# Performance work log

Measured on AMD Instinct MI355X. Metric: run time of the kernel, lower is better.

Reference implementation:

```python
import jax, jax.numpy as jnp
import numpy as np

EMBED_DIM = 1024
NUM_HEADS = 16
HEAD_DIM = EMBED_DIM // NUM_HEADS


def setup_inputs() -> dict:
    key = jax.random.key(0)
    k1, k2, k3, k4, k5 = jax.random.split(key, 5)
    B, T, C = 2, 2048, EMBED_DIM
    s = 1.0 / np.sqrt(C)
    return {
        "x": jax.random.normal(k1, (B, T, C), dtype=jnp.float32),
        "W_qkv": jax.random.normal(k2, (C, 3 * C), dtype=jnp.float32) * s,
        "b_qkv": jnp.zeros((3 * C,), dtype=jnp.float32),
        "W_out": jax.random.normal(k3, (C, C), dtype=jnp.float32) * s,
        "b_out": jnp.zeros((C,), dtype=jnp.float32),
    }


def reference(x, W_qkv, b_qkv, W_out, b_out):
    B, T, C = x.shape
    H, D = NUM_HEADS, HEAD_DIM
    qkv = x @ W_qkv + b_qkv                       # [B, T, 3C]
    q, k, v = jnp.split(qkv, 3, axis=-1)
    # [B, H, T, D]
    q = q.reshape(B, T, H, D).transpose(0, 2, 1, 3)
    k = k.reshape(B, T, H, D).transpose(0, 2, 1, 3)
    v = v.reshape(B, T, H, D).transpose(0, 2, 1, 3)
    scores = jnp.einsum("bhqd,bhkd->bhqk", q, k) / np.sqrt(D)  # [B,H,T,T]
    causal = jnp.tril(jnp.ones((T, T), dtype=bool))
    scores = jnp.where(causal[None, None], scores, -jnp.inf)
    weights = jax.nn.softmax(scores, axis=-1)
    out = jnp.einsum("bhqk,bhkd->bhqd", weights, v)  # [B,H,T,D]
    out = out.transpose(0, 2, 1, 3).reshape(B, T, C)
    return out @ W_out + b_out
```

## Files before the change

### kernel.cpp

```cpp
#include <hip/hip_runtime.h>
#include <stdint.h>

typedef unsigned short u16t;
typedef __attribute__((ext_vector_type(8))) short bf16x8;
typedef __attribute__((ext_vector_type(4))) float f32x4;

#define DEV __device__ __forceinline__

DEV u16t f2bf(float f) {
  union { float f; unsigned u; } v; v.f = f;
  unsigned r = v.u + 0x7FFFu + ((v.u >> 16) & 1u);
  return (u16t)(r >> 16);
}

DEV unsigned cvtpk(float a, float b) {
  unsigned r;
  asm("v_cvt_pk_bf16_f32 %0, %1, %2" : "=v"(r) : "v"(a), "v"(b));
  return r;
}

DEV void glds16(const void* g, void* l) {
  __builtin_amdgcn_global_load_lds((const __attribute__((address_space(1))) void*)g,
                                   (__attribute__((address_space(3))) void*)l, 16, 0, 0);
}

DEV void transpose_tile(const float* __restrict__ src, u16t* __restrict__ dst,
                        int R, int C, int c0, int r0, u16t (*tile)[65]) {
  int tid = threadIdx.x;
#pragma unroll
  for (int i = 0; i < 16; i++) {
    int idx = tid + i * 256;
    int r = idx >> 6, c = idx & 63;
    tile[c][r] = f2bf(src[(size_t)(r0 + r) * C + (c0 + c)]);
  }
  __syncthreads();
#pragma unroll
  for (int i = 0; i < 16; i++) {
    int idx = tid + i * 256;
    int rr = idx >> 6, cc = idx & 63;
    dst[(size_t)(c0 + rr) * R + (r0 + cc)] = tile[rr][cc];
  }
}

__global__ __launch_bounds__(256) void k_prep(const float* __restrict__ x,
                                              u16t* __restrict__ xb,
                                              const float* __restrict__ Wqkv,
                                              u16t* __restrict__ wqkvT,
                                              const float* __restrict__ Wout,
                                              u16t* __restrict__ woutT) {
  __shared__ u16t tile[64][65];
  const int bid = blockIdx.x;
  if (bid < 2048) {
    int i = (bid * 256 + threadIdx.x) * 8;
    const float4* p = (const float4*)(x + i);
    float4 a = p[0], b = p[1];
    union { u16t h[8]; int4 v; } o;
    o.h[0] = f2bf(a.x); o.h[1] = f2bf(a.y); o.h[2] = f2bf(a.z); o.h[3] = f2bf(a.w);
    o.h[4] = f2bf(b.x); o.h[5] = f2bf(b.y); o.h[6] = f2bf(b.z); o.h[7] = f2bf(b.w);
    *(int4*)(xb + i) = o.v;
  } else if (bid < 2816) {
    int b2 = bid - 2048;
    transpose_tile(Wqkv, wqkvT, 1024, 3072, (b2 % 48) * 64, (b2 / 48) * 64, tile);
  } else {
    int b3 = bid - 2816;
    transpose_tile(Wout, woutT, 1024, 1024, (b3 & 15) * 64, (b3 >> 4) * 64, tile);
  }
}

template <int K, int BM, int BN>
DEV void gemm_mainloop_t(const u16t* __restrict__ A, const u16t* __restrict__ Bt,
                         int m0, int n0, u16t* ldsA, u16t* ldsB,
                         f32x4 (&acc)[BM / 32][BN / 32]) {
  constexpr int MF = BM / 32, NF = BN / 32;
  const int tid = threadIdx.x;
  const int lane = tid & 63;
  const int wid = tid >> 6;
  const int wm = wid >> 1, wn = wid & 1;
#pragma unroll
  for (int i = 0; i < MF; i++)
#pragma unroll
    for (int j = 0; j < NF; j++) acc[i][j] = f32x4{0.f, 0.f, 0.f, 0.f};

  char* lA = (char*)ldsA;
  char* lB = (char*)ldsB;

  for (int k0 = 0; k0 < K; k0 += 32) {
#pragma unroll
    for (int j = wid; j < BM / 16; j += 4) {
      int g = j * 64 + lane;
      int row = g >> 2;
      int cb = (g & 3) * 16;
      glds16((const char*)(A + (size_t)(m0 + row) * K + k0) + cb, lA + j * 1024);
    }
#pragma unroll
    for (int j = wid; j < BN / 16; j += 4) {
      int g = j * 64 + lane;
      int row = g >> 2;
      int cb = (g & 3) * 16;
      glds16((const char*)(Bt + (size_t)(n0 + row) * K + k0) + cb, lB + j * 1024);
    }
    __syncthreads();
    bf16x8 af[MF], bfr[NF];
    const int lr = lane & 15;
    const int ko = (lane >> 4) * 8;
#pragma unroll
    for (int f = 0; f < MF; f++)
      af[f] = *(const bf16x8*)(ldsA + (wm * (BM / 2) + f * 16 + lr) * 32 + ko);
#pragma unroll
    for (int f = 0; f < NF; f++)
      bfr[f] = *(const bf16x8*)(ldsB + (wn * (BN / 2) + f * 16 + lr) * 32 + ko);
#pragma unroll
    for (int i = 0; i < MF; i++)
#pragma unroll
      for (int j = 0; j < NF; j++)
        acc[i][j] = __builtin_amdgcn_mfma_f32_16x16x32_bf16(af[i], bfr[j], acc[i][j], 0, 0, 0);
    __syncthreads();
  }
}

__global__ __launch_bounds__(256) void k_gemm_qkv(const u16t* __restrict__ xb,
                                                  const u16t* __restrict__ wt,
                                                  const float* __restrict__ bias,
                                                  u16t* __restrict__ q,
                                                  u16t* __restrict__ kk,
                                                  u16t* __restrict__ vt) {
  __shared__ alignas(16) char pool[32768];
  u16t* ldsA = (u16t*)pool;
  u16t* ldsB = (u16t*)(pool + 8192);
  const int m0 = blockIdx.x * 128, n0 = blockIdx.y * 128;
  f32x4 acc[4][4];
  gemm_mainloop_t<1024, 128, 128>(xb, wt, m0, n0, ldsA, ldsB, acc);

  const int lane = threadIdx.x & 63, wid = threadIdx.x >> 6;
  const int wm = wid >> 1, wn = wid & 1;
  const int nbase = n0 + wn * 64;
  const int which = nbase >> 10;
  const int hb = (nbase & 1023) >> 6;
  const int bb = m0 >> 11;
  const int t0 = (m0 & 2047) + wm * 64;
  const int bh = bb * 16 + hb;
  u16t* eb = (u16t*)(pool + wid * 8192);
#pragma unroll
  for (int fm = 0; fm < 4; fm++) {
#pragma unroll
    for (int fn = 0; fn < 4; fn++) {
      float bv = bias[nbase + fn * 16 + (lane & 15)];
#pragma unroll
      for (int i = 0; i < 4; i++) {
        int t_loc = fm * 16 + (lane >> 4) * 4 + i;
        int d_loc = fn * 16 + (lane & 15);
        float v = acc[fm][fn][i] + bv;
        if (which == 2) eb[d_loc * 64 + t_loc] = f2bf(v);
        else            eb[t_loc * 64 + d_loc] = f2bf(v);
      }
    }
  }
  asm volatile("s_waitcnt lgkmcnt(0)" ::: "memory");
  u16t* dst;
  size_t base, rowstride;
  if (which == 2) { dst = vt; base = (size_t)bh * 64 * 2048 + t0; rowstride = 2048; }
  else { dst = (which == 0) ? q : kk; base = ((size_t)bh * 2048 + t0) * 64; rowstride = 64; }
#pragma unroll
  for (int it = 0; it < 8; it++) {
    int g = it * 64 + lane;
    int r = g >> 3;
    int ce = (g & 7) * 8;
    *(int4*)(dst + base + (size_t)r * rowstride + ce) = *(const int4*)(eb + r * 64 + ce);
  }
}

__global__ __launch_bounds__(128) void k_attn(const u16t* __restrict__ q,
                                              const u16t* __restrict__ kk,
                                              const u16t* __restrict__ vt,
                                              u16t* __restrict__ attn) {
  __shared__ u16t ldsK[64 * 64];
  __shared__ u16t ldsV[64 * 64];
  __shared__ u16t ldsP[2][16 * 64];
  const int lin = blockIdx.x;
  const int swz = (lin & 7) * 128 + (lin >> 3);
  const int p = swz & 31;
  const int bh = swz >> 5;
  const int t_lo = p, t_hi = 63 - p;
  const int lo_last = t_lo >> 1, hi_last = t_hi >> 1;
  const int tid = threadIdx.x;
  const int lane = tid & 63, wid = tid >> 6;
  const int lr = lane & 15, lg = lane >> 4;
  const size_t hbase = (size_t)bh * 2048 * 64;
  const size_t vbase = (size_t)bh * 64 * 2048;
  const float NINF = -__builtin_inff();
  const float CEXP = 0.1803368801111204f;
  const float NMC  = -48.0f * 0.1803368801111204f;

  bf16x8 qlo[2], qhi[2];
  {
    const u16t* qp  = q + hbase + (size_t)(t_lo * 32 + wid * 16 + lr) * 64 + lg * 8;
    const u16t* qp2 = q + hbase + (size_t)(t_hi * 32 + wid * 16 + lr) * 64 + lg * 8;
#pragma unroll
    for (int ks = 0; ks < 2; ks++) {
      qlo[ks] = *(const bf16x8*)(qp + ks * 32);
      qhi[ks] = *(const bf16x8*)(qp2 + ks * 32);
    }
  }

  f32x4 olo[4], ohi[4];
#pragma unroll
  for (int i = 0; i < 4; i++) {
    olo[i] = f32x4{0.f, 0.f, 0.f, 0.f};
    ohi[i] = f32x4{0.f, 0.f, 0.f, 0.f};
  }
  float llo = 0.f, lhi = 0.f;

  u16t* pb = ldsP[wid];

  auto stage = [&](int kt) {
#pragma unroll
    for (int j = 0; j < 4; j++) {
      int g = j * 128 + tid;
      int r = g >> 3;
      int cb = (g & 7) * 16;
      int sc = cb ^ ((r & 7) << 4);
      glds16((const char*)(kk + hbase + (size_t)(kt * 64 + r) * 64) + sc,
             (char*)ldsK + j * 2048 + wid * 1024);
      glds16((const char*)(vt + vbase + (size_t)r * 2048 + kt * 64) + sc,
             (char*)ldsV + j * 2048 + wid * 1024);
    }
  };

  auto compute = [&](bool diag, int moff, const bf16x8* qf, f32x4* o, float& l_part) {
    const char* K = (const char*)ldsK;
    const char* V = (const char*)ldsV;
    float sv[4][4];
    __builtin_amdgcn_s_setprio(1);
#pragma unroll
    for (int f = 0; f < 4; f++) {
      f32x4 s = f32x4{0.f, 0.f, 0.f, 0.f};
#pragma unroll
      for (int ks = 0; ks < 2; ks++) {
        int row = f * 16 + lr;
        int cb = ks * 64 + lg * 16;
        bf16x8 kf = *(const bf16x8*)(K + row * 128 + (cb ^ ((row & 7) << 4)));
        s = __builtin_amdgcn_mfma_f32_16x16x32_bf16(kf, qf[ks], s, 0, 0, 0);
      }
#pragma unroll
      for (int i = 0; i < 4; i++) sv[f][i] = s[i];
    }
    __builtin_amdgcn_s_setprio(0);
    if (diag) {
      int qr = moff + wid * 16 + lr;
#pragma unroll
      for (int f = 0; f < 4; f++)
#pragma unroll
        for (int i = 0; i < 4; i++)
          if (f * 16 + lg * 4 + i > qr) sv[f][i] = NINF;
    }
    float ps[4][4];
    float fs[4];
#pragma unroll
    for (int f = 0; f < 4; f++) {
#pragma unroll
      for (int i = 0; i < 4; i++)
        ps[f][i] = exp2f(__builtin_fmaf(sv[f][i], CEXP, NMC));
      fs[f] = (ps[f][0] + ps[f][1]) + (ps[f][2] + ps[f][3]);
    }
    l_part += (fs[0] + fs[1]) + (fs[2] + fs[3]);
#pragma unroll
    for (int f = 0; f < 4; f++) {
      union { unsigned u[2]; uint2 v; } pk;
      pk.u[0] = cvtpk(ps[f][0], ps[f][1]);
      pk.u[1] = cvtpk(ps[f][2], ps[f][3]);
      int cby = (f * 32 + lg * 8) ^ ((lr & 7) << 4);
      *(uint2*)((char*)pb + lr * 128 + cby) = pk.v;
    }
    asm volatile("s_waitcnt lgkmcnt(0)" ::: "memory");
    __builtin_amdgcn_s_setprio(1);
#pragma unroll
    for (int ks = 0; ks < 2; ks++) {
      int cb = ks * 64 + lg * 16;
      bf16x8 pf = *(const bf16x8*)((const char*)pb + lr * 128 + (cb ^ ((lr & 7) << 4)));
#pragma unroll
      for (int df = 0; df < 4; df++) {
        int vrow = df * 16 + lr;
        bf16x8 vf = *(const bf16x8*)(V + vrow * 128 + (cb ^ ((vrow & 7) << 4)));
        o[df] = __builtin_amdgcn_mfma_f32_16x16x32_bf16(vf, pf, o[df], 0, 0, 0);
      }
    }
    __builtin_amdgcn_s_setprio(0);
  };

  for (int kt = 0; kt <= hi_last; kt++) {
    stage(kt);
    __syncthreads();
    compute(kt == hi_last, (t_hi & 1) << 5, qhi, ohi, lhi);
    if (kt <= lo_last) compute(kt == lo_last, (t_lo & 1) << 5, qlo, olo, llo);
    __syncthreads();
  }

  const int bb = bh >> 4, h = bh & 15;
  auto epi = [&](int qt, const f32x4* o, float l_part) {
    float l = l_part;
    l += __shfl_xor(l, 16);
    l += __shfl_xor(l, 32);
    float rinv = 1.0f / l;
    int t = qt * 32 + wid * 16 + lr;
    size_t rowb = ((size_t)bb * 2048 + t) * 1024 + h * 64;
#pragma unroll
    for (int df = 0; df < 4; df++) {
      union { unsigned u[2]; uint2 v; } pk;
      pk.u[0] = cvtpk(o[df][0] * rinv, o[df][1] * rinv);
      pk.u[1] = cvtpk(o[df][2] * rinv, o[df][3] * rinv);
      *(uint2*)(attn + rowb + df * 16 + lg * 4) = pk.v;
    }
  };
  epi(t_lo, olo, llo);
  epi(t_hi, ohi, lhi);
}

__global__ __launch_bounds__(256) void k_gemm_out(const u16t* __restrict__ attn,
                                                  const u16t* __restrict__ wt,
                                                  const float* __restrict__ bias,
                                                  float* __restrict__ out) {
  __shared__ u16t ldsA[64 * 32];
  __shared__ u16t ldsB[128 * 32];
  const int m0 = blockIdx.x * 64, n0 = blockIdx.y * 128;
  f32x4 acc[2][4];
  gemm_mainloop_t<1024, 64, 128>(attn, wt, m0, n0, ldsA, ldsB, acc);

  const int lane = threadIdx.x & 63, wid = threadIdx.x >> 6;
  const int wm = wid >> 1, wn = wid & 1;
#pragma unroll
  for (int fm = 0; fm < 2; fm++) {
    int row = m0 + wm * 32 + fm * 16 + (lane >> 4) * 4;
#pragma unroll
    for (int fn = 0; fn < 4; fn++) {
      int col = n0 + wn * 64 + fn * 16 + (lane & 15);
      float bv = bias[col];
#pragma unroll
      for (int i = 0; i < 4; i++)
        out[(size_t)(row + i) * 1024 + col] = acc[fm][fn][i] + bv;
    }
  }
}

extern "C" void kernel_launch(void* const* d_in, const int* in_sizes, int n_in,
                              void* d_out, int out_size, void* d_ws, size_t ws_size,
                              hipStream_t stream) {
  const float* x     = (const float*)d_in[0];
  const float* W_qkv = (const float*)d_in[1];
  const float* b_qkv = (const float*)d_in[2];
  const float* W_out = (const float*)d_in[3];
  const float* b_out = (const float*)d_in[4];
  float* out = (float*)d_out;

  char* ws = (char*)d_ws;
  u16t* xb    = (u16t*)(ws);
  u16t* wqkvT = (u16t*)(ws + 8388608);
  u16t* woutT = (u16t*)(ws + 14680064);
  u16t* qb    = (u16t*)(ws + 16777216);
  u16t* kb    = (u16t*)(ws + 25165824);
  u16t* vtb   = (u16t*)(ws + 33554432);
  u16t* attnb = (u16t*)(ws + 41943040);

  k_prep<<<3072, 256, 0, stream>>>(x, xb, W_qkv, wqkvT, W_out, woutT);
  k_gemm_qkv<<<dim3(32, 24), 256, 0, stream>>>(xb, wqkvT, b_qkv, qb, kb, vtb);
  k_attn<<<1024, 128, 0, stream>>>(qb, kb, vtb, attnb);
  k_gemm_out<<<dim3(64, 8), 256, 0, stream>>>(attnb, woutT, b_out, out);
}
```

Measured before the change: 118.5 us.

## Use single-wave attention blocks with 16-row query tiles and no block barriers

The attention kernel moves from 128-thread blocks, where two waves share each staged K/V tile, to 64-thread single-wave blocks that each own two 16-row query tiles paired for causal load balance. The grid doubles to 2048 blocks. With one wave per block, __syncthreads is replaced by a vmcnt wait, which removes barrier stalls. In exchange, each block loads the full K/V tiles for only 16 query rows, which doubles K/V staging traffic per query row and removes the data reuse across waves.

```diff
diff --git a/kernel.cpp b/kernel.cpp
--- a/kernel.cpp
+++ b/kernel.cpp
@@ -169,21 +169,20 @@
   }
 }
 
-__global__ __launch_bounds__(128) void k_attn(const u16t* __restrict__ q,
-                                              const u16t* __restrict__ kk,
-                                              const u16t* __restrict__ vt,
-                                              u16t* __restrict__ attn) {
+__global__ __launch_bounds__(64) void k_attn(const u16t* __restrict__ q,
+                                             const u16t* __restrict__ kk,
+                                             const u16t* __restrict__ vt,
+                                             u16t* __restrict__ attn) {
   __shared__ u16t ldsK[64 * 64];
   __shared__ u16t ldsV[64 * 64];
-  __shared__ u16t ldsP[2][16 * 64];
+  __shared__ u16t ldsP[16 * 64];
   const int lin = blockIdx.x;
-  const int swz = (lin & 7) * 128 + (lin >> 3);
-  const int p = swz & 31;
-  const int bh = swz >> 5;
-  const int t_lo = p, t_hi = 63 - p;
-  const int lo_last = t_lo >> 1, hi_last = t_hi >> 1;
-  const int tid = threadIdx.x;
-  const int lane = tid & 63, wid = tid >> 6;
+  const int swz = (lin & 7) * 256 + (lin >> 3);
+  const int bh = swz >> 6;
+  const int pr = swz & 63;
+  const int t_lo = pr, t_hi = 127 - pr;
+  const int lo_last = t_lo >> 2, hi_last = t_hi >> 2;
+  const int lane = threadIdx.x;
   const int lr = lane & 15, lg = lane >> 4;
   const size_t hbase = (size_t)bh * 2048 * 64;
   const size_t vbase = (size_t)bh * 64 * 2048;
@@ -193,8 +192,8 @@
 
   bf16x8 qlo[2], qhi[2];
   {
-    const u16t* qp  = q + hbase + (size_t)(t_lo * 32 + wid * 16 + lr) * 64 + lg * 8;
-    const u16t* qp2 = q + hbase + (size_t)(t_hi * 32 + wid * 16 + lr) * 64 + lg * 8;
+    const u16t* qp  = q + hbase + (size_t)(t_lo * 16 + lr) * 64 + lg * 8;
+    const u16t* qp2 = q + hbase + (size_t)(t_hi * 16 + lr) * 64 + lg * 8;
 #pragma unroll
     for (int ks = 0; ks < 2; ks++) {
       qlo[ks] = *(const bf16x8*)(qp + ks * 32);
@@ -210,19 +209,17 @@
   }
   float llo = 0.f, lhi = 0.f;
 
-  u16t* pb = ldsP[wid];
-
   auto stage = [&](int kt) {
 #pragma unroll
-    for (int j = 0; j < 4; j++) {
-      int g = j * 128 + tid;
+    for (int j = 0; j < 8; j++) {
+      int g = j * 64 + lane;
       int r = g >> 3;
       int cb = (g & 7) * 16;
       int sc = cb ^ ((r & 7) << 4);
       glds16((const char*)(kk + hbase + (size_t)(kt * 64 + r) * 64) + sc,
-             (char*)ldsK + j * 2048 + wid * 1024);
+             (char*)ldsK + j * 1024);
       glds16((const char*)(vt + vbase + (size_t)r * 2048 + kt * 64) + sc,
-             (char*)ldsV + j * 2048 + wid * 1024);
+             (char*)ldsV + j * 1024);
     }
   };
 
@@ -246,7 +243,7 @@
     }
     __builtin_amdgcn_s_setprio(0);
     if (diag) {
-      int qr = moff + wid * 16 + lr;
+      int qr = moff + lr;
 #pragma unroll
       for (int f = 0; f < 4; f++)
 #pragma unroll
@@ -269,14 +266,14 @@
       pk.u[0] = cvtpk(ps[f][0], ps[f][1]);
       pk.u[1] = cvtpk(ps[f][2], ps[f][3]);
       int cby = (f * 32 + lg * 8) ^ ((lr & 7) << 4);
-      *(uint2*)((char*)pb + lr * 128 + cby) = pk.v;
+      *(uint2*)((char*)ldsP + lr * 128 + cby) = pk.v;
     }
     asm volatile("s_waitcnt lgkmcnt(0)" ::: "memory");
     __builtin_amdgcn_s_setprio(1);
 #pragma unroll
     for (int ks = 0; ks < 2; ks++) {
       int cb = ks * 64 + lg * 16;
-      bf16x8 pf = *(const bf16x8*)((const char*)pb + lr * 128 + (cb ^ ((lr & 7) << 4)));
+      bf16x8 pf = *(const bf16x8*)((const char*)ldsP + lr * 128 + (cb ^ ((lr & 7) << 4)));
 #pragma unroll
       for (int df = 0; df < 4; df++) {
         int vrow = df * 16 + lr;
@@ -289,10 +286,9 @@
 
   for (int kt = 0; kt <= hi_last; kt++) {
     stage(kt);
-    __syncthreads();
-    compute(kt == hi_last, (t_hi & 1) << 5, qhi, ohi, lhi);
-    if (kt <= lo_last) compute(kt == lo_last, (t_lo & 1) << 5, qlo, olo, llo);
-    __syncthreads();
+    asm volatile("s_waitcnt vmcnt(0)" ::: "memory");
+    compute(kt == hi_last, (t_hi & 3) << 4, qhi, ohi, lhi);
+    if (kt <= lo_last) compute(kt == lo_last, (t_lo & 3) << 4, qlo, olo, llo);
   }
 
   const int bb = bh >> 4, h = bh & 15;
@@ -301,7 +297,7 @@
     l += __shfl_xor(l, 16);
     l += __shfl_xor(l, 32);
     float rinv = 1.0f / l;
-    int t = qt * 32 + wid * 16 + lr;
+    int t = qt * 16 + lr;
     size_t rowb = ((size_t)bb * 2048 + t) * 1024 + h * 64;
 #pragma unroll
     for (int df = 0; df < 4; df++) {
@@ -362,6 +358,6 @@
 
   k_prep<<<3072, 256, 0, stream>>>(x, xb, W_qkv, wqkvT, W_out, woutT);
   k_gemm_qkv<<<dim3(32, 24), 256, 0, stream>>>(xb, wqkvT, b_qkv, qb, kb, vtb);
-  k_attn<<<1024, 128, 0, stream>>>(qb, kb, vtb, attnb);
+  k_attn<<<2048, 64, 0, stream>>>(qb, kb, vtb, attnb);
   k_gemm_out<<<dim3(64, 8), 256, 0, stream>>>(attnb, woutT, b_out, out);
 }
```

Result: slower. 124.7 us (+5.2%).
